# Performance work log

Hardware: AMD Instinct MI355X
Metric: run time of the kernel (lower is better)

The kernel has to match this reference:

```python
import jax, jax.numpy as jnp
import numpy as np

SH_C0 = 0.28209479177387814
EPS2D = 0.3      # gsplat low-pass filter added to 2D covariance diagonal
NEAR = 0.01
ALPHA_MIN = 1.0 / 255.0
ALPHA_MAX = 0.999


def setup_inputs() -> dict:
    key = jax.random.key(0)
    ks = jax.random.split(key, 5)
    N = 2048
    means = 0.1 * jax.random.normal(ks[0], (N, 3), jnp.float32)
    quats = jax.random.normal(ks[1], (N, 4), jnp.float32)
    scales = -2.3 + 0.3 * jax.random.normal(ks[2], (N, 3), jnp.float32)
    opacities = -1.0 + 0.5 * jax.random.normal(ks[3], (N,), jnp.float32)
    sh_coeffs = jax.random.normal(ks[4], (N, 1, 3), jnp.float32)
    viewmats = jnp.eye(4, dtype=jnp.float32).at[2, 3].set(2.0)[None]  # [1,4,4] world->cam
    Ks = jnp.array([[[150.0, 0.0, 64.0], [0.0, 150.0, 64.0], [0.0, 0.0, 1.0]]], jnp.float32)
    return dict(means=means, quats=quats, scales=scales, opacities=opacities,
                sh_coeffs=sh_coeffs, viewmats=viewmats, Ks=Ks, width=128, height=128)


def _splat_render(means, quats, scales, opacities, sh_coeffs, viewmats, Ks, width, height):
    # --- parameter activations (GaussianSplat.activated_parameters) ---
    quats = quats / jnp.linalg.norm(quats, axis=-1, keepdims=True)
    scales = jnp.minimum(jnp.exp(scales), 10.0)
    opac = jax.nn.sigmoid(opacities)                                  # [N]
    colors = jnp.maximum(sh_coeffs[:, 0, :] * SH_C0 + 0.5, 0.0)       # [N,3] sh_degree=0

    # --- 3D covariance from quaternion (w,x,y,z) and scale ---
    w, x, y, z = quats[:, 0], quats[:, 1], quats[:, 2], quats[:, 3]
    R = jnp.stack([
        1 - 2 * (y * y + z * z), 2 * (x * y - w * z), 2 * (x * z + w * y),
        2 * (x * y + w * z), 1 - 2 * (x * x + z * z), 2 * (y * z - w * x),
        2 * (x * z - w * y), 2 * (y * z + w * x), 1 - 2 * (x * x + y * y)],
        axis=-1).reshape(-1, 3, 3)                                    # [N,3,3]
    M = R * scales[:, None, :]                                        # R @ diag(s)
    cov3d = jnp.einsum('nij,nkj->nik', M, M)                          # [N,3,3]

    # --- project to camera frame ---
    Rcw = viewmats[:, :3, :3]                                         # [C,3,3]
    tcw = viewmats[:, :3, 3]                                          # [C,3]
    p_cam = jnp.einsum('cij,nj->cni', Rcw, means) + tcw[:, None, :]   # [C,N,3]
    Vc = jnp.einsum('cij,njk,clk->cnil', Rcw, cov3d, Rcw)             # [C,N,3,3]

    xc, yc, zc = p_cam[..., 0], p_cam[..., 1], p_cam[..., 2]
    valid = zc > NEAR
    zs = jnp.where(valid, zc, 1.0)
    rz = 1.0 / zs
    fx = Ks[:, 0, 0][:, None]; fy = Ks[:, 1, 1][:, None]
    cx = Ks[:, 0, 2][:, None]; cy = Ks[:, 1, 2][:, None]
    u = fx * xc * rz + cx                                             # [C,N]
    v = fy * yc * rz + cy

    # --- EWA 2D covariance: J Vc J^T + eps2d*I, J = d(proj)/d(p_cam) ---
    J00 = fx * rz; J02 = -fx * xc * rz * rz
    J11 = fy * rz; J12 = -fy * yc * rz * rz
    V00, V01, V02 = Vc[..., 0, 0], Vc[..., 0, 1], Vc[..., 0, 2]
    V11, V12, V22 = Vc[..., 1, 1], Vc[..., 1, 2], Vc[..., 2, 2]
    a = J00 * J00 * V00 + 2 * J00 * J02 * V02 + J02 * J02 * V22 + EPS2D
    b = J00 * (J11 * V01 + J12 * V02) + J02 * (J11 * V12 + J12 * V22)
    c = J11 * J11 * V11 + 2 * J11 * J12 * V12 + J12 * J12 * V22 + EPS2D
    det = a * c - b * b
    valid = valid & (det > 0)
    det_s = jnp.where(valid, det, 1.0)
    conA = c / det_s; conB = -b / det_s; conC = a / det_s             # conic (inverse cov)

    # --- per-pixel gaussian evaluation (pixel centers at +0.5) ---
    px = jnp.arange(width, dtype=jnp.float32) + 0.5                   # [W]
    py = jnp.arange(height, dtype=jnp.float32) + 0.5                  # [H]
    dx = px[None, None, :] - u[..., None]                             # [C,N,W]
    dy = py[None, None, :] - v[..., None]                             # [C,N,H]
    sigma = (0.5 * (conA[..., None, None] * (dx * dx)[:, :, None, :]
                    + conC[..., None, None] * (dy * dy)[..., None])
             + conB[..., None, None] * dy[..., None] * dx[:, :, None, :])  # [C,N,H,W]
    alpha = opac[None, :, None, None] * jnp.exp(-sigma)
    alpha = jnp.minimum(alpha, ALPHA_MAX)
    alpha = jnp.where(valid[..., None, None] & (alpha >= ALPHA_MIN), alpha, 0.0)

    # --- front-to-back alpha compositing in depth order ---
    order = jnp.argsort(jnp.where(valid, zc, jnp.inf), axis=1)        # [C,N]
    alpha_s = jnp.take_along_axis(alpha, order[:, :, None, None], axis=1)
    colors_s = jnp.take_along_axis(jnp.broadcast_to(colors[None], (alpha.shape[0],) + colors.shape),
                                   order[:, :, None], axis=1)         # [C,N,3]
    logT = jnp.cumsum(jnp.log1p(-alpha_s), axis=1)
    logT_excl = jnp.pad(logT, ((0, 0), (1, 0), (0, 0), (0, 0)))[:, :-1]
    weights = alpha_s * jnp.exp(logT_excl)                            # [C,N,H,W]
    img = jnp.einsum('cnhw,cnk->chwk', weights, colors_s)             # [C,H,W,3]
    return img


def reference(means, quats, scales, opacities, sh_coeffs, viewmats, Ks, width, height):
    return _splat_render(means, quats, scales, opacities, sh_coeffs, viewmats, Ks, width, height)
```

## Files before the change

### kernel.cpp

```cpp
#include <hip/hip_runtime.h>
#include <math.h>

#define SH_C0     0.28209479177387814f
#define EPS2D     0.3f
#define NEARZ     0.01f
#define ALPHA_MIN (1.0f/255.0f)
#define ALPHA_MAX 0.999f
#define LOG2E     1.4426950408889634f

#define NSEG   16
#define MAXN   2048

__global__ __launch_bounds__(256) void prep_rank_kernel(
        const float* __restrict__ means,
        const float* __restrict__ quats,
        const float* __restrict__ scales,
        const float* __restrict__ opacities,
        const float* __restrict__ sh,
        const float* __restrict__ vm,
        const float* __restrict__ K,
        float* __restrict__ sorted,
        int N) {
    int wave = blockIdx.x * 4 + (threadIdx.x >> 6);
    int lane = threadIdx.x & 63;
    if (wave >= N) return;
    int i = wave;

    float r00=vm[0], r01=vm[1], r02=vm[2],  t0=vm[3];
    float r10=vm[4], r11=vm[5], r12=vm[6],  t1=vm[7];
    float r20=vm[8], r21=vm[9], r22=vm[10], t2=vm[11];

    float mx = means[3*i+0], my = means[3*i+1], mz = means[3*i+2];
    float zci = r20*mx + r21*my + r22*mz + t2;
    float keyi = (zci > NEARZ) ? zci : INFINITY;
    int cnt = 0;
    for (int j = lane; j < N; j += 64) {
        float ax = means[3*j+0], ay = means[3*j+1], az = means[3*j+2];
        float zcj = r20*ax + r21*ay + r22*az + t2;
        float keyj = (zcj > NEARZ) ? zcj : INFINITY;
        cnt += (keyj < keyi) || (keyj == keyi && j < i);
    }
    #pragma unroll
    for (int off = 32; off > 0; off >>= 1)
        cnt += __shfl_xor(cnt, off, 64);

    float qw = quats[4*i+0], qx = quats[4*i+1], qy = quats[4*i+2], qz = quats[4*i+3];
    float rqn = rsqrtf(qw*qw + qx*qx + qy*qy + qz*qz);
    qw *= rqn; qx *= rqn; qy *= rqn; qz *= rqn;

    float R00 = 1.f - 2.f*(qy*qy + qz*qz);
    float R01 = 2.f*(qx*qy - qw*qz);
    float R02 = 2.f*(qx*qz + qw*qy);
    float R10 = 2.f*(qx*qy + qw*qz);
    float R11 = 1.f - 2.f*(qx*qx + qz*qz);
    float R12 = 2.f*(qy*qz - qw*qx);
    float R20 = 2.f*(qx*qz - qw*qy);
    float R21 = 2.f*(qy*qz + qw*qx);
    float R22 = 1.f - 2.f*(qx*qx + qy*qy);

    float s0 = fminf(expf(scales[3*i+0]), 10.f);
    float s1 = fminf(expf(scales[3*i+1]), 10.f);
    float s2 = fminf(expf(scales[3*i+2]), 10.f);

    float M00=R00*s0, M01=R01*s1, M02=R02*s2;
    float M10=R10*s0, M11=R11*s1, M12=R12*s2;
    float M20=R20*s0, M21=R21*s1, M22=R22*s2;

    float c00 = M00*M00 + M01*M01 + M02*M02;
    float c01 = M00*M10 + M01*M11 + M02*M12;
    float c02 = M00*M20 + M01*M21 + M02*M22;
    float c11 = M10*M10 + M11*M11 + M12*M12;
    float c12 = M10*M20 + M11*M21 + M12*M22;
    float c22 = M20*M20 + M21*M21 + M22*M22;

    float xc = r00*mx + r01*my + r02*mz + t0;
    float yc = r10*mx + r11*my + r12*mz + t1;
    float zc = zci;

    float T00 = r00*c00 + r01*c01 + r02*c02;
    float T01 = r00*c01 + r01*c11 + r02*c12;
    float T02 = r00*c02 + r01*c12 + r02*c22;
    float T10 = r10*c00 + r11*c01 + r12*c02;
    float T11 = r10*c01 + r11*c11 + r12*c12;
    float T12 = r10*c02 + r11*c12 + r12*c22;
    float T20 = r20*c00 + r21*c01 + r22*c02;
    float T21 = r20*c01 + r21*c11 + r22*c12;
    float T22 = r20*c02 + r21*c12 + r22*c22;
    float V00 = T00*r00 + T01*r01 + T02*r02;
    float V01 = T00*r10 + T01*r11 + T02*r12;
    float V02 = T00*r20 + T01*r21 + T02*r22;
    float V11 = T10*r10 + T11*r11 + T12*r12;
    float V12 = T10*r20 + T11*r21 + T12*r22;
    float V22 = T20*r20 + T21*r21 + T22*r22;

    float fx = K[0], cx = K[2], fy = K[4], cy = K[5];

    bool valid = zc > NEARZ;
    float zs = valid ? zc : 1.0f;
    float rz = 1.0f / zs;
    float u = fx*xc*rz + cx;
    float v = fy*yc*rz + cy;
    float J00 = fx*rz;
    float J02 = -fx*xc*rz*rz;
    float J11 = fy*rz;
    float J12 = -fy*yc*rz*rz;

    float a = J00*J00*V00 + 2.f*J00*J02*V02 + J02*J02*V22 + EPS2D;
    float b = J00*(J11*V01 + J12*V02) + J02*(J11*V12 + J12*V22);
    float c = J11*J11*V11 + 2.f*J11*J12*V12 + J12*J12*V22 + EPS2D;
    float det = a*c - b*b;
    valid = valid && (det > 0.f);
    float det_s = valid ? det : 1.0f;
    float conA =  c / det_s;
    float conB = -b / det_s;
    float conC =  a / det_s;

    float op  = 1.0f / (1.0f + expf(-opacities[i]));
    float cr = fmaxf(sh[3*i+0]*SH_C0 + 0.5f, 0.f);
    float cg = fmaxf(sh[3*i+1]*SH_C0 + 0.5f, 0.f);
    float cb = fmaxf(sh[3*i+2]*SH_C0 + 0.5f, 0.f);

    float smax = logf(op * 255.0f);
    bool vis = valid && (smax > 0.f);
    float denom = conA*conC - conB*conB;
    float rxe = 0.f, rye = 0.f;
    float uu = -1.0e9f, vv = -1.0e9f;
    float e4 = 0.f, e5 = 0.f, e6 = 0.f, e7 = 0.f;
    if (vis) {
        float inv = 2.f * smax / denom;
        rxe = sqrtf(fmaxf(inv * conC, 0.f)) + 0.5f;
        rye = sqrtf(fmaxf(inv * conA, 0.f)) + 0.5f;
        uu = u; vv = v;
        e4 = 0.5f*conA*LOG2E; e5 = conB*LOG2E; e6 = 0.5f*conC*LOG2E; e7 = op;
    }

    if (lane < 12) {
        float val;
        switch (lane) {
            case 0:  val = uu;  break;
            case 1:  val = vv;  break;
            case 2:  val = rxe; break;
            case 3:  val = rye; break;
            case 4:  val = e4;  break;
            case 5:  val = e5;  break;
            case 6:  val = e6;  break;
            case 7:  val = e7;  break;
            case 8:  val = cr;  break;
            case 9:  val = cg;  break;
            case 10: val = cb;  break;
            default: val = 0.f; break;
        }
        sorted[12*(size_t)cnt + lane] = val;
    }
}

__global__ __launch_bounds__(1024, 4) void render_tile_kernel(
        const float4* __restrict__ rec,
        float* __restrict__ out,
        int N) {
    __shared__ unsigned long long masks[(MAXN + 63) / 64];
    __shared__ int cnts[NSEG];
    __shared__ unsigned short list[MAXN];
    __shared__ float4 part[NSEG][64];

    int tid  = threadIdx.x;
    int lane = tid & 63;
    int w    = tid >> 6;
    int t    = blockIdx.x;
    int tx   = (t & 15) << 3;
    int ty   = (t >> 4) << 3;

    float tcx = (float)tx + 4.0f;
    float tcy = (float)ty + 4.0f;
    float px  = (float)(tx + (lane & 7)) + 0.5f;
    float py  = (float)(ty + (lane >> 3)) + 0.5f;

    int nwords = (N + 63) >> 6;
    int wpw    = (nwords + NSEG - 1) / NSEG;
    int w0     = w * wpw;
    int w1     = min(w0 + wpw, nwords);

    int mycnt = 0;
    for (int word = w0; word < w1; ++word) {
        int g = (word << 6) + lane;
        bool hit = false;
        if (g < N) {
            float4 r0 = rec[3*(size_t)g];
            hit = (fabsf(r0.x - tcx) <= r0.z + 3.5f) &&
                  (fabsf(r0.y - tcy) <= r0.w + 3.5f);
        }
        unsigned long long m = __ballot(hit);
        if (lane == 0) masks[word] = m;
        mycnt += (int)__popcll(m);
    }
    if (lane == 0) cnts[w] = mycnt;
    __syncthreads();

    int off = 0, L = 0;
    #pragma unroll
    for (int s = 0; s < NSEG; ++s) {
        int cs = cnts[s];
        if (s < w) off += cs;
        L += cs;
    }
    unsigned long long lt = (1ull << lane) - 1ull;
    for (int word = w0; word < w1; ++word) {
        unsigned long long m = masks[word];
        bool hit = (m >> lane) & 1ull;
        int p = (int)__popcll(m & lt);
        if (hit) list[off + p] = (unsigned short)((word << 6) + lane);
        off += (int)__popcll(m);
    }
    __syncthreads();

    int chunk = (L + NSEG - 1) / NSEG;
    int i0 = w * chunk;
    int i1 = min(i0 + chunk, L);

    float accr = 0.f, accg = 0.f, accb = 0.f, T = 1.f;
    for (int i = i0; i < i1; ++i) {
        int idx = (int)list[i];
        idx = __builtin_amdgcn_readfirstlane(idx);
        const float4* r = rec + 3*(size_t)idx;
        float4 r0 = r[0];
        float4 r1 = r[1];
        float4 r2 = r[2];
        float dx = px - r0.x, dy = py - r0.y;
        float tt  = fmaf(r1.x, dx, r1.y * dy);
        float arg = fmaf(-r1.z, dy*dy, -dx*tt);
        float al  = r1.w * __builtin_amdgcn_exp2f(arg);
        al = fminf(al, ALPHA_MAX);
        al = (al >= ALPHA_MIN) ? al : 0.f;
        float wg = T * al;
        accr = fmaf(wg, r2.x, accr);
        accg = fmaf(wg, r2.y, accg);
        accb = fmaf(wg, r2.z, accb);
        T = fmaf(-al, T, T);
        if (__all(T < 1e-9f)) break;
    }
    part[w][lane] = make_float4(accr, accg, accb, T);
    __syncthreads();

    if (tid < 64) {
        float R = 0.f, G = 0.f, B = 0.f, Tr = 1.f;
        #pragma unroll
        for (int s = 0; s < NSEG; ++s) {
            float4 q = part[s][tid];
            R  = fmaf(Tr, q.x, R);
            G  = fmaf(Tr, q.y, G);
            B  = fmaf(Tr, q.z, B);
            Tr *= q.w;
        }
        int x = tx + (tid & 7);
        int y = ty + (tid >> 3);
        int p = y * 128 + x;
        out[3*(size_t)p+0] = R;
        out[3*(size_t)p+1] = G;
        out[3*(size_t)p+2] = B;
    }
}

extern "C" void kernel_launch(void* const* d_in, const int* in_sizes, int n_in,
                              void* d_out, int out_size, void* d_ws, size_t ws_size,
                              hipStream_t stream) {
    const float* means     = (const float*)d_in[0];
    const float* quats     = (const float*)d_in[1];
    const float* scales    = (const float*)d_in[2];
    const float* opacities = (const float*)d_in[3];
    const float* sh        = (const float*)d_in[4];
    const float* vm        = (const float*)d_in[5];
    const float* K         = (const float*)d_in[6];

    int N = in_sizes[0] / 3;

    float* sorted = (float*)d_ws;

    prep_rank_kernel<<<(N + 3) / 4, 256, 0, stream>>>(
        means, quats, scales, opacities, sh, vm, K, sorted, N);
    render_tile_kernel<<<256, 1024, 0, stream>>>(
        (const float4*)sorted, (float*)d_out, N);
}
```

Baseline: 106.8 us.

## Split bbox into compact array, fold opacity into exponent, repack render record

```diff
diff --git a/kernel.cpp b/kernel.cpp
--- a/kernel.cpp
+++ b/kernel.cpp
@@ -19,7 +19,8 @@
         const float* __restrict__ sh,
         const float* __restrict__ vm,
         const float* __restrict__ K,
-        float* __restrict__ sorted,
+        float* __restrict__ rec,
+        float* __restrict__ bbox,
         int N) {
     int wave = blockIdx.x * 4 + (threadIdx.x >> 6);
     int lane = threadIdx.x & 63;
@@ -123,39 +124,46 @@
     float smax = logf(op * 255.0f);
     bool vis = valid && (smax > 0.f);
     float denom = conA*conC - conB*conB;
-    float rxe = 0.f, rye = 0.f;
     float uu = -1.0e9f, vv = -1.0e9f;
-    float e4 = 0.f, e5 = 0.f, e6 = 0.f, e7 = 0.f;
+    float rxp = 0.f, ryp = 0.f;
+    float e2 = 0.f, e3 = 0.f, e4 = 0.f, e5 = -1.0e4f;
     if (vis) {
         float inv = 2.f * smax / denom;
-        rxe = sqrtf(fmaxf(inv * conC, 0.f)) + 0.5f;
-        rye = sqrtf(fmaxf(inv * conA, 0.f)) + 0.5f;
+        rxp = sqrtf(fmaxf(inv * conC, 0.f)) + 4.0f;
+        ryp = sqrtf(fmaxf(inv * conA, 0.f)) + 4.0f;
         uu = u; vv = v;
-        e4 = 0.5f*conA*LOG2E; e5 = conB*LOG2E; e6 = 0.5f*conC*LOG2E; e7 = op;
-    }
-
-    if (lane < 12) {
+        e2 = 0.5f*conA*LOG2E; e3 = conB*LOG2E; e4 = 0.5f*conC*LOG2E;
+        e5 = log2f(op);
+    }
+
+    if (lane < 16) {
         float val;
         switch (lane) {
             case 0:  val = uu;  break;
             case 1:  val = vv;  break;
-            case 2:  val = rxe; break;
-            case 3:  val = rye; break;
+            case 2:  val = e2;  break;
+            case 3:  val = e3;  break;
             case 4:  val = e4;  break;
             case 5:  val = e5;  break;
-            case 6:  val = e6;  break;
-            case 7:  val = e7;  break;
-            case 8:  val = cr;  break;
-            case 9:  val = cg;  break;
-            case 10: val = cb;  break;
-            default: val = 0.f; break;
+            case 6:  val = cr;  break;
+            case 7:  val = cg;  break;
+            case 8:  val = cb;  break;
+            case 9:  val = 0.f; break;
+            case 10: val = 0.f; break;
+            case 11: val = 0.f; break;
+            case 12: val = uu;  break;
+            case 13: val = vv;  break;
+            case 14: val = rxp; break;
+            default: val = ryp; break;
         }
-        sorted[12*(size_t)cnt + lane] = val;
+        if (lane < 12) rec[12*(size_t)cnt + lane] = val;
+        else           bbox[4*(size_t)cnt + (lane - 12)] = val;
     }
 }
 
 __global__ __launch_bounds__(1024, 4) void render_tile_kernel(
         const float4* __restrict__ rec,
+        const float4* __restrict__ bbox,
         float* __restrict__ out,
         int N) {
     __shared__ unsigned long long masks[(MAXN + 63) / 64];
@@ -185,9 +193,9 @@
         int g = (word << 6) + lane;
         bool hit = false;
         if (g < N) {
-            float4 r0 = rec[3*(size_t)g];
-            hit = (fabsf(r0.x - tcx) <= r0.z + 3.5f) &&
-                  (fabsf(r0.y - tcy) <= r0.w + 3.5f);
+            float4 bb = bbox[g];
+            hit = (fabsf(bb.x - tcx) <= bb.z) &&
+                  (fabsf(bb.y - tcy) <= bb.w);
         }
         unsigned long long m = __ballot(hit);
         if (lane == 0) masks[word] = m;
@@ -214,29 +222,29 @@
     __syncthreads();
 
     int chunk = (L + NSEG - 1) / NSEG;
-    int i0 = w * chunk;
+    int i0 = min(w * chunk, L);
     int i1 = min(i0 + chunk, L);
 
     float accr = 0.f, accg = 0.f, accb = 0.f, T = 1.f;
+    #pragma unroll 2
     for (int i = i0; i < i1; ++i) {
-        int idx = (int)list[i];
-        idx = __builtin_amdgcn_readfirstlane(idx);
+        int idx = __builtin_amdgcn_readfirstlane((int)list[i]);
         const float4* r = rec + 3*(size_t)idx;
         float4 r0 = r[0];
         float4 r1 = r[1];
         float4 r2 = r[2];
         float dx = px - r0.x, dy = py - r0.y;
-        float tt  = fmaf(r1.x, dx, r1.y * dy);
-        float arg = fmaf(-r1.z, dy*dy, -dx*tt);
-        float al  = r1.w * __builtin_amdgcn_exp2f(arg);
+        float tt  = fmaf(r0.z, dx, r0.w * dy);
+        float arg = fmaf(-r1.x, dy*dy, r1.y);
+        arg = fmaf(-dx, tt, arg);
+        float al  = __builtin_amdgcn_exp2f(arg);
         al = fminf(al, ALPHA_MAX);
         al = (al >= ALPHA_MIN) ? al : 0.f;
         float wg = T * al;
-        accr = fmaf(wg, r2.x, accr);
-        accg = fmaf(wg, r2.y, accg);
-        accb = fmaf(wg, r2.z, accb);
+        accr = fmaf(wg, r1.z, accr);
+        accg = fmaf(wg, r1.w, accg);
+        accb = fmaf(wg, r2.x, accb);
         T = fmaf(-al, T, T);
-        if (__all(T < 1e-9f)) break;
     }
     part[w][lane] = make_float4(accr, accg, accb, T);
     __syncthreads();
@@ -273,10 +281,11 @@
 
     int N = in_sizes[0] / 3;
 
-    float* sorted = (float*)d_ws;
+    float* rec  = (float*)d_ws;
+    float* bbox = rec + (size_t)N * 12;
 
     prep_rank_kernel<<<(N + 3) / 4, 256, 0, stream>>>(
-        means, quats, scales, opacities, sh, vm, K, sorted, N);
+        means, quats, scales, opacities, sh, vm, K, rec, bbox, N);
     render_tile_kernel<<<256, 1024, 0, stream>>>(
-        (const float4*)sorted, (float*)d_out, N);
+        (const float4*)rec, (const float4*)bbox, (float*)d_out, N);
 }
```

Measured after the change: 108.5 us. Within noise of the previous version (+1.6%).
